# Performance work log

Hardware: AMD Instinct MI355X
Metric: run time of the kernel (lower is better)

The kernel has to match this reference:

```python
import jax, jax.numpy as jnp
import numpy as np

N, E, B = 50000, 800000, 64
IN_DIM, HID = 128, 64
H1 = 2  # heads in gat1
NEG_SLOPE = 0.2


def _glorot(key, shape):
    fan_in = shape[0]
    return jax.random.normal(key, shape, dtype=jnp.float32) / jnp.sqrt(jnp.float32(fan_in))


def setup_inputs() -> dict:
    key = jax.random.key(0)
    ks = jax.random.split(key, 24)
    x = jax.random.normal(ks[0], (N, IN_DIM), dtype=jnp.float32)
    edge_index = jax.random.randint(ks[1], (2, E), 0, N, dtype=jnp.int64)
    batch = jnp.sort(jax.random.randint(ks[2], (N,), 0, B, dtype=jnp.int64))
    d = {
        'x': x, 'edge_index': edge_index, 'batch': batch,
        # gat1: in=128 -> heads=2, out=64 (concat -> 128)
        'w1_l': _glorot(ks[3], (IN_DIM, H1 * HID)), 'b1_l': jnp.zeros((H1 * HID,), jnp.float32),
        'w1_r': _glorot(ks[4], (IN_DIM, H1 * HID)), 'b1_r': jnp.zeros((H1 * HID,), jnp.float32),
        'att1': _glorot(ks[5], (H1, HID)), 'bias1': jnp.zeros((H1 * HID,), jnp.float32),
        # gat2: in=128 -> heads=1, out=64
        'w2_l': _glorot(ks[6], (H1 * HID, HID)), 'b2_l': jnp.zeros((HID,), jnp.float32),
        'w2_r': _glorot(ks[7], (H1 * HID, HID)), 'b2_r': jnp.zeros((HID,), jnp.float32),
        'att2': _glorot(ks[8], (1, HID)), 'bias2': jnp.zeros((HID,), jnp.float32),
        # gate_nn: Linear(64,64) -> ReLU -> Linear(64,1)
        'gate_w1': _glorot(ks[9], (HID, HID)), 'gate_b1': jnp.zeros((HID,), jnp.float32),
        'gate_w2': _glorot(ks[10], (HID, 1)), 'gate_b2': jnp.zeros((1,), jnp.float32),
        # MLP head
        'lin1_w': _glorot(ks[11], (HID, HID)), 'lin1_b': jnp.zeros((HID,), jnp.float32),
        'lin2_w': _glorot(ks[12], (HID, 1)), 'lin2_b': jnp.zeros((1,), jnp.float32),
    }
    return d


def _segment_softmax(scores, seg, num_segments):
    # scores: [E, H]; softmax over edges sharing the same seg id (per column)
    m = jax.ops.segment_max(scores, seg, num_segments=num_segments)
    m = jnp.where(jnp.isfinite(m), m, 0.0)
    ex = jnp.exp(scores - m[seg])
    s = jax.ops.segment_sum(ex, seg, num_segments=num_segments)
    return ex / (s[seg] + 1e-16)


def _gatv2(x, src, dst, w_l, b_l, w_r, b_r, att, bias, heads, out_dim, n_nodes):
    xl = (x @ w_l + b_l).reshape(n_nodes, heads, out_dim)
    xr = (x @ w_r + b_r).reshape(n_nodes, heads, out_dim)
    e = jax.nn.leaky_relu(xl[src] + xr[dst], NEG_SLOPE)      # [E,H,D]
    score = jnp.einsum('ehd,hd->eh', e, att)                  # [E,H]
    alpha = _segment_softmax(score, dst, n_nodes)             # [E,H]
    out = jax.ops.segment_sum(alpha[..., None] * xl[src], dst, num_segments=n_nodes)
    return out.reshape(n_nodes, heads * out_dim) + bias


def reference(x, edge_index, batch, w1_l, b1_l, w1_r, b1_r, att1, bias1,
              w2_l, b2_l, w2_r, b2_r, att2, bias2,
              gate_w1, gate_b1, gate_w2, gate_b2,
              lin1_w, lin1_b, lin2_w, lin2_b):
    n = x.shape[0]
    # PyG GATv2Conv default add_self_loops=True
    loop = jnp.arange(n, dtype=edge_index.dtype)
    src = jnp.concatenate([edge_index[0], loop])
    dst = jnp.concatenate([edge_index[1], loop])

    h = jax.nn.relu(_gatv2(x, src, dst, w1_l, b1_l, w1_r, b1_r, att1, bias1, H1, HID, n))
    h = jax.nn.relu(_gatv2(h, src, dst, w2_l, b2_l, w2_r, b2_r, att2, bias2, 1, HID, n))

    # GlobalAttention pool: gate = gate_nn(h); softmax over batch; weighted sum
    gate = jax.nn.relu(h @ gate_w1 + gate_b1) @ gate_w2 + gate_b2     # [N,1]
    alpha = _segment_softmax(gate, batch, B)                           # [N,1]
    pooled = jax.ops.segment_sum(alpha * h, batch, num_segments=B)     # [B,HID]

    out = jax.nn.relu(pooled @ lin1_w + lin1_b)
    out = (out @ lin2_w + lin2_b).squeeze(-1)                          # [B]
    return out
```

## Files before the change

kernel.cpp:

```cpp
#include <hip/hip_runtime.h>

typedef float v2f __attribute__((ext_vector_type(2)));
typedef float v4f __attribute__((ext_vector_type(4)));
typedef _Float16 h4 __attribute__((ext_vector_type(4)));
typedef _Float16 f16x8 __attribute__((ext_vector_type(8)));

template<int N> struct IC { static constexpr int value = N; };


__global__ void k_init(const float* __restrict__ w1_l, const float* __restrict__ w1_r,
                       const float* __restrict__ b1_l, const float* __restrict__ b1_r,
                       const float* __restrict__ w2_l, const float* __restrict__ w2_r,
                       const float* __restrict__ b2_l, const float* __restrict__ b2_r,
                       _Float16* __restrict__ wc1h, _Float16* __restrict__ wc1l,
                       _Float16* __restrict__ wc2h, _Float16* __restrict__ wc2l,
                       float* __restrict__ bc1, float* __restrict__ bc2,
                       int* __restrict__ deg, int n){
  int i = blockIdx.x*256 + threadIdx.x;
  if (i < n) deg[i] = 0;
  if (i < 256*128){
    int col = i >> 7, k = i & 127;
    float v = (col < 128) ? w1_l[k*128 + col] : w1_r[k*128 + (col - 128)];
    _Float16 h = (_Float16)v;
    wc1h[i] = h; wc1l[i] = (_Float16)(v - (float)h);
  }
  if (i < 128*128){
    int col = i >> 7, k = i & 127;
    float v = (col < 64) ? w2_l[k*64 + col] : w2_r[k*64 + (col - 64)];
    _Float16 h = (_Float16)v;
    wc2h[i] = h; wc2l[i] = (_Float16)(v - (float)h);
  }
  if (i < 256) bc1[i] = (i < 128) ? b1_l[i] : b1_r[i - 128];
  if (i < 128) bc2[i] = (i < 64)  ? b2_l[i] : b2_r[i - 64];
}

__global__ void k_hist(const int* __restrict__ dstp, int* __restrict__ deg, int E){
  int e = blockIdx.x*256 + threadIdx.x;
  if (e < E) atomicAdd(&deg[dstp[e]], 1);
}

__global__ void k_scan1(const int* __restrict__ deg, int* __restrict__ rowptr,
                        int* __restrict__ bsum, int n){
  __shared__ int s[256];
  int i = blockIdx.x*256 + threadIdx.x;
  int v = (i < n) ? deg[i] + 1 : 0;
  s[threadIdx.x] = v;
  __syncthreads();
  for (int off = 1; off < 256; off <<= 1){
    int t = (threadIdx.x >= off) ? s[threadIdx.x - off] : 0;
    __syncthreads();
    s[threadIdx.x] += t;
    __syncthreads();
  }
  if (i < n) rowptr[i] = s[threadIdx.x] - v;
  if (threadIdx.x == 255) bsum[blockIdx.x] = s[255];
}

__global__ void k_scan2(int* bsum, int nb){
  __shared__ int s[256];
  int v = (threadIdx.x < nb) ? bsum[threadIdx.x] : 0;
  s[threadIdx.x] = v;
  __syncthreads();
  for (int off = 1; off < 256; off <<= 1){
    int t = (threadIdx.x >= off) ? s[threadIdx.x - off] : 0;
    __syncthreads();
    s[threadIdx.x] += t;
    __syncthreads();
  }
  if (threadIdx.x < nb) bsum[threadIdx.x] = s[threadIdx.x] - v;
}

__global__ void k_scan3(int* rowptr, const int* __restrict__ bsum,
                        int* __restrict__ srcs, int* __restrict__ cursor,
                        int n, int total){
  int i = blockIdx.x*256 + threadIdx.x;
  if (i < n){
    int b = rowptr[i] + bsum[blockIdx.x];
    rowptr[i] = b;
    srcs[b] = i;
    cursor[i] = b + 1;
  }
  if (i == 0) rowptr[n] = total;
}

__global__ void k_scatter(const int* __restrict__ srcp, const int* __restrict__ dstp,
                          int* __restrict__ cursor, int* __restrict__ srcs, int E){
  int e = blockIdx.x*256 + threadIdx.x;
  if (e < E){
    int p = atomicAdd(&cursor[dstp[e]], 1);
    srcs[p] = srcp[e];
  }
}


#define MBM 64
#define MBN 128
#define MBK 32

__device__ __forceinline__ int lds_idx(int row, int k){
  return row*32 + ((((k >> 3) ^ row) & 3) << 3) + (k & 7);
}

__global__ __launch_bounds__(256) void k_gemm_mfma(
    const float* __restrict__ A, const _Float16* __restrict__ Wh,
    const _Float16* __restrict__ Wl, const float* __restrict__ bias,
    _Float16* __restrict__ Cxl, float* __restrict__ Cxr,
    int M, int K, int N, int xlCols){
  __shared__ _Float16 Ah[MBM*MBK], Al[MBM*MBK];
  __shared__ _Float16 Bh[MBN*MBK], Bl[MBN*MBK];
  int bm = blockIdx.x * MBM, bn = blockIdx.y * MBN;
  int tid = threadIdx.x;
  int lane = tid & 63, wv = tid >> 6;
  v4f acc[8] = {};
  const int fragoff = (lane & 15)*32 + ((((lane >> 4) ^ lane) & 3) << 3);
  for (int k0 = 0; k0 < K; k0 += MBK){
    #pragma unroll
    for (int l = 0; l < 2; l++){
      int idx = tid + l*256;
      int r = idx >> 3, kq = (idx & 7) * 4;
      float4 v = make_float4(0.f, 0.f, 0.f, 0.f);
      if (bm + r < M) v = *(const float4*)(A + (size_t)(bm + r)*K + k0 + kq);
      _Float16 e0 = (_Float16)v.x, e1 = (_Float16)v.y,
               e2 = (_Float16)v.z, e3 = (_Float16)v.w;
      h4 hh = {e0, e1, e2, e3};
      h4 ll = {(_Float16)(v.x - (float)e0), (_Float16)(v.y - (float)e1),
               (_Float16)(v.z - (float)e2), (_Float16)(v.w - (float)e3)};
      int o = lds_idx(r, kq);
      *(h4*)(&Ah[o]) = hh;
      *(h4*)(&Al[o]) = ll;
    }
    #pragma unroll
    for (int l = 0; l < 2; l++){
      int idx = tid + l*256;
      int c = idx >> 2, kc = (idx & 3) * 8;
      size_t go = (size_t)(bn + c)*K + k0 + kc;
      int o = lds_idx(c, kc);
      *(f16x8*)(&Bh[o]) = *(const f16x8*)(Wh + go);
      *(f16x8*)(&Bl[o]) = *(const f16x8*)(Wl + go);
    }
    __syncthreads();
    f16x8 ah = *(const f16x8*)(&Ah[wv*16*32 + fragoff]);
    f16x8 al = *(const f16x8*)(&Al[wv*16*32 + fragoff]);
    #pragma unroll
    for (int t = 0; t < 8; t++){
      f16x8 bh = *(const f16x8*)(&Bh[t*16*32 + fragoff]);
      f16x8 bl = *(const f16x8*)(&Bl[t*16*32 + fragoff]);
      acc[t] = __builtin_amdgcn_mfma_f32_16x16x32_f16(ah, bh, acc[t], 0, 0, 0);
      acc[t] = __builtin_amdgcn_mfma_f32_16x16x32_f16(ah, bl, acc[t], 0, 0, 0);
      acc[t] = __builtin_amdgcn_mfma_f32_16x16x32_f16(al, bh, acc[t], 0, 0, 0);
    }
    __syncthreads();
  }
  int rbase = bm + wv*16 + (lane >> 4)*4;
  int cl = lane & 15;
  int NR = N - xlCols;
  #pragma unroll
  for (int t = 0; t < 8; t++){
    int col = bn + t*16 + cl;
    float bv = bias[col];
    bool isXl = (bn + t*16) < xlCols;
    #pragma unroll
    for (int i = 0; i < 4; i++){
      int r = rbase + i;
      if (r < M){
        float o = acc[t][i] + bv;
        if (isXl) Cxl[(size_t)r*xlCols + col] = (_Float16)o;
        else      Cxr[(size_t)r*NR + (col - xlCols)] = o;
      }
    }
  }
}


template<int CTRL>
__device__ __forceinline__ float dpp_add(float x){
  int t = __builtin_amdgcn_update_dpp(0, __float_as_int(x), CTRL, 0xf, 0xf, true);
  return x + __int_as_float(t);
}


template<int H>
__global__ __launch_bounds__(256) void k_gat_fused(
    const _Float16* __restrict__ xlh, const float* __restrict__ xr,
    const int* __restrict__ rowptr, const int* __restrict__ srcs,
    const float* __restrict__ att, const float* __restrict__ bias,
    float* __restrict__ out, int n){
  int gid = blockIdx.x * blockDim.x + threadIdx.x;
  int nd = gid >> 6, lane = gid & 63;
  if (nd >= n) return;
  constexpr int SHIFTB = (H == 2) ? 8 : 7;
  constexpr int EPI = (H == 2) ? 2 : 4;
  const int q = lane & 15;
  const int hsel = (H == 2) ? ((lane >> 4) & 1) : 0;
  const int elane = (H == 2) ? (lane >> 5) : (lane >> 4);
  const int fpos = hsel*64 + q*4;
  const unsigned foff = (unsigned)fpos * 2u;
  const char* __restrict__ xbase = (const char*)xlh;
  v4f xrv = *(const v4f*)(xr + (size_t)nd*(H*64) + fpos);
  v4f av  = *(const v4f*)(att + fpos);
  v4f acc = {0.f, 0.f, 0.f, 0.f};
  float den = 0.f;
  int s0 = rowptr[nd], s1 = rowptr[nd+1];
  for (int base = s0; base < s1; base += 64){
    int idx = base + lane;
    int sv = (idx < s1) ? srcs[idx] : 0;
    int cnt = min(64, s1 - base);
    auto batchU = [&](int i, auto Uc, bool full){
      constexpr int U = decltype(Uc)::value;
      int aidx[U];
      h4 hv[U];
      #pragma unroll
      for (int u = 0; u < U; u++)
        aidx[u] = __builtin_amdgcn_ds_bpermute((i + u*EPI + elane) << 2, sv);
      #pragma unroll
      for (int u = 0; u < U; u++)
        hv[u] = *(const h4*)(xbase + (((unsigned)aidx[u] << SHIFTB) + foff));
      #pragma unroll
      for (int u = 0; u < U; u++){
        v4f xv = {(float)hv[u].x, (float)hv[u].y, (float)hv[u].z, (float)hv[u].w};
        v4f t  = xv + xrv;
        v4f lt = __builtin_elementwise_max(t, t * 0.2f);
        v4f pr = lt * av;
        float p = (pr.x + pr.y) + (pr.z + pr.w);
        p = dpp_add<0x111>(p);
        p = dpp_add<0x112>(p);
        p = dpp_add<0x114>(p);
        p = dpp_add<0x118>(p);
        p = __int_as_float(__builtin_amdgcn_ds_swizzle(__float_as_int(p), 0x1F0));
        float ex = __expf(p);
        if (!full) ex = (elane < cnt - (i + u*EPI)) ? ex : 0.f;
        den += ex;
        acc += xv * ex;
      }
    };
    int i = 0;
    for (; i + 8*EPI <= cnt; i += 8*EPI) batchU(i, IC<8>{}, true);
    if (i + 4*EPI <= cnt){ batchU(i, IC<4>{}, true); i += 4*EPI; }
    if (i + 2*EPI <= cnt){ batchU(i, IC<2>{}, true); i += 2*EPI; }
    for (; i < cnt; i += EPI) batchU(i, IC<1>{}, i + EPI <= cnt);
  }
  if (H == 1){
    den   += __shfl_xor(den,   16, 64);
    acc.x += __shfl_xor(acc.x, 16, 64);
    acc.y += __shfl_xor(acc.y, 16, 64);
    acc.z += __shfl_xor(acc.z, 16, 64);
    acc.w += __shfl_xor(acc.w, 16, 64);
  }
  den   += __shfl_xor(den,   32, 64);
  acc.x += __shfl_xor(acc.x, 32, 64);
  acc.y += __shfl_xor(acc.y, 32, 64);
  acc.z += __shfl_xor(acc.z, 32, 64);
  acc.w += __shfl_xor(acc.w, 32, 64);
  if (lane < 16*H){
    v4f bv = *(const v4f*)(bias + lane*4);
    float inv = 1.f / (den + 1e-16f);
    v4f o = acc * inv + bv;
    v4f z = {0.f, 0.f, 0.f, 0.f};
    o = __builtin_elementwise_max(o, z);
    *(v4f*)(out + (size_t)nd*(H*64) + lane*4) = o;
  }
}


__global__ __launch_bounds__(256) void k_gate(
    const float* __restrict__ h2, const float* __restrict__ gw1,
    const float* __restrict__ gb1, const float* __restrict__ gw2,
    const float* __restrict__ gb2, float* __restrict__ exn, int M){
  __shared__ float As[32][64 + 4];
  __shared__ float Ws[32][64];
  int bm = blockIdx.x * 64;
  int tid = threadIdx.x;
  int tx = tid & 15, ty = tid >> 4;
  float acc[4][4] = {};
  for (int k0 = 0; k0 < 64; k0 += 32){
    #pragma unroll
    for (int l = 0; l < 2; l++){
      int idx = tid + l*256;
      int r = idx >> 3, c4 = (idx & 7) * 4;
      float4 v = make_float4(0.f, 0.f, 0.f, 0.f);
      if (bm + r < M) v = *(const float4*)(h2 + (size_t)(bm + r)*64 + k0 + c4);
      As[c4+0][r] = v.x; As[c4+1][r] = v.y; As[c4+2][r] = v.z; As[c4+3][r] = v.w;
      int kr = idx >> 4, wc4 = (idx & 15) * 4;
      *(float4*)(&Ws[kr][wc4]) = *(const float4*)(gw1 + (size_t)(k0 + kr)*64 + wc4);
    }
    __syncthreads();
    #pragma unroll
    for (int k = 0; k < 32; k++){
      float4 a4 = *(const float4*)(&As[k][ty*4]);
      float4 w4 = *(const float4*)(&Ws[k][tx*4]);
      float av[4] = {a4.x, a4.y, a4.z, a4.w};
      float wv[4] = {w4.x, w4.y, w4.z, w4.w};
      #pragma unroll
      for (int i = 0; i < 4; i++)
        #pragma unroll
        for (int j = 0; j < 4; j++)
          acc[i][j] = fmaf(av[i], wv[j], acc[i][j]);
    }
    __syncthreads();
  }
  float4 b4 = *(const float4*)(gb1 + tx*4);
  float4 w2 = *(const float4*)(gw2 + tx*4);
  float gb2v = gb2[0];
  #pragma unroll
  for (int i = 0; i < 4; i++){
    float p = fmaxf(acc[i][0] + b4.x, 0.f) * w2.x;
    p = fmaf(fmaxf(acc[i][1] + b4.y, 0.f), w2.y, p);
    p = fmaf(fmaxf(acc[i][2] + b4.z, 0.f), w2.z, p);
    p = fmaf(fmaxf(acc[i][3] + b4.w, 0.f), w2.w, p);
    p = dpp_add<0x111>(p);
    p = dpp_add<0x112>(p);
    p = dpp_add<0x114>(p);
    p = dpp_add<0x118>(p);
    if (tx == 15){
      int r = bm + ty*4 + i;
      if (r < M) exn[r] = __expf(p + gb2v);
    }
  }
}


__global__ __launch_bounds__(1024) void k_pool_mlp(
    const float* __restrict__ h2, const float* __restrict__ exn,
    const int* __restrict__ batch, int n,
    const float* __restrict__ l1w, const float* __restrict__ l1b,
    const float* __restrict__ l2w, const float* __restrict__ l2b,
    float* __restrict__ out){
  __shared__ float accs[16][64];
  __shared__ float dens[16];
  int b = blockIdx.x;
  int tid = threadIdx.x, lane = tid & 63, wv = tid >> 6;
  int lo = 0, hi = n;
  while (lo < hi){ int m = (lo + hi) >> 1; if (batch[m] < b) lo = m + 1; else hi = m; }
  int start = lo;
  hi = n;
  while (lo < hi){ int m = (lo + hi) >> 1; if (batch[m] < b + 1) lo = m + 1; else hi = m; }
  int end = lo;
  float acc = 0.f, den = 0.f;
  for (int nd = start + wv; nd < end; nd += 16){
    float ex = exn[nd];
    den += ex;
    acc = fmaf(ex, h2[(size_t)nd*64 + lane], acc);
  }
  accs[wv][lane] = acc;
  if (lane == 0) dens[wv] = den;
  __syncthreads();
  if (wv == 0){
    float p = 0.f, d = 0.f;
    #pragma unroll
    for (int w = 0; w < 16; w++){ p += accs[w][lane]; d += dens[w]; }
    p = p / (d + 1e-16f);
    float t = l1b[lane];
    #pragma unroll
    for (int k = 0; k < 64; k++)
      t = fmaf(__shfl(p, k, 64), l1w[k*64 + lane], t);
    t = fmaxf(t, 0.f) * l2w[lane];
    #pragma unroll
    for (int off = 32; off; off >>= 1) t += __shfl_xor(t, off, 64);
    if (lane == 0) out[b] = t + l2b[0];
  }
}


extern "C" void kernel_launch(void* const* d_in, const int* in_sizes, int n_in,
                              void* d_out, int out_size, void* d_ws, size_t ws_size,
                              hipStream_t stream){
  const float* x    = (const float*)d_in[0];
  const int*   ei   = (const int*)  d_in[1];
  const int*   batch= (const int*)  d_in[2];
  const float* w1_l = (const float*)d_in[3];  const float* b1_l = (const float*)d_in[4];
  const float* w1_r = (const float*)d_in[5];  const float* b1_r = (const float*)d_in[6];
  const float* att1 = (const float*)d_in[7];  const float* bias1= (const float*)d_in[8];
  const float* w2_l = (const float*)d_in[9];  const float* b2_l = (const float*)d_in[10];
  const float* w2_r = (const float*)d_in[11]; const float* b2_r = (const float*)d_in[12];
  const float* att2 = (const float*)d_in[13]; const float* bias2= (const float*)d_in[14];
  const float* gw1  = (const float*)d_in[15]; const float* gb1  = (const float*)d_in[16];
  const float* gw2  = (const float*)d_in[17]; const float* gb2  = (const float*)d_in[18];
  const float* l1w  = (const float*)d_in[19]; const float* l1b  = (const float*)d_in[20];
  const float* l2w  = (const float*)d_in[21]; const float* l2b  = (const float*)d_in[22];

  const int n = in_sizes[0] / 128;
  const int E = in_sizes[1] / 2;
  const int Bb = out_size;
  const int Etot = E + n;
  const int* srcp = ei;
  const int* dstp = ei + E;

  char* wsbase = (char*)d_ws;
  size_t off = 0;
  auto alloc = [&](size_t bytes)->char*{
    char* p = wsbase + off;
    off = (off + bytes + 255) & ~(size_t)255;
    return p;
  };
  int*   deg    = (int*)  alloc((size_t)n*4);
  int*   rowptr = (int*)  alloc((size_t)(n+1)*4);
  int*   cursor = (int*)  alloc((size_t)n*4);
  int*   bsum   = (int*)  alloc(1024);
  int*   srcs   = (int*)  alloc((size_t)Etot*4);
  _Float16* wc1h = (_Float16*)alloc(256*128*2);
  _Float16* wc1l = (_Float16*)alloc(256*128*2);
  _Float16* wc2h = (_Float16*)alloc(128*128*2);
  _Float16* wc2l = (_Float16*)alloc(128*128*2);
  float* bc1    = (float*)alloc(256*4);
  float* bc2    = (float*)alloc(128*4);
  _Float16* xlh1 = (_Float16*)alloc((size_t)n*128*2);
  float* xr1    = (float*)alloc((size_t)n*128*4);
  float* h1     = (float*)alloc((size_t)n*128*4);
  _Float16* xlh2 = xlh1;
  float* xr2 = xr1;
  float* h2  = xr1 + (size_t)n*64;
  float* exn = h1;

  int nb = (n + 255) / 256;
  int eb = (E + 255) / 256;
  int ib = (((n > 32768) ? n : 32768) + 255) / 256;

  k_init<<<ib, 256, 0, stream>>>(w1_l, w1_r, b1_l, b1_r, w2_l, w2_r, b2_l, b2_r,
                                 wc1h, wc1l, wc2h, wc2l, bc1, bc2, deg, n);
  k_hist<<<eb, 256, 0, stream>>>(dstp, deg, E);
  k_scan1<<<nb, 256, 0, stream>>>(deg, rowptr, bsum, n);
  k_scan2<<<1, 256, 0, stream>>>(bsum, nb);
  k_scan3<<<nb, 256, 0, stream>>>(rowptr, bsum, srcs, cursor, n, Etot);
  k_scatter<<<eb, 256, 0, stream>>>(srcp, dstp, cursor, srcs, E);

  dim3 g1((n + MBM - 1)/MBM, 2);
  k_gemm_mfma<<<g1, 256, 0, stream>>>(x, wc1h, wc1l, bc1, xlh1, xr1, n, 128, 256, 128);
  long long thr = (long long)n * 64;
  int gatb = (int)((thr + 255)/256);
  k_gat_fused<2><<<gatb, 256, 0, stream>>>(xlh1, xr1, rowptr, srcs, att1, bias1, h1, n);

  dim3 g2((n + MBM - 1)/MBM, 1);
  k_gemm_mfma<<<g2, 256, 0, stream>>>(h1, wc2h, wc2l, bc2, xlh2, xr2, n, 128, 128, 64);
  k_gat_fused<1><<<gatb, 256, 0, stream>>>(xlh2, xr2, rowptr, srcs, att2, bias2, h2, n);

  k_gate<<<(n + 63)/64, 256, 0, stream>>>(h2, gw1, gb1, gw2, gb2, exn, n);

  k_pool_mlp<<<Bb, 1024, 0, stream>>>(h2, exn, batch, n, l1w, l1b, l2w, l2b, (float*)d_out);
}
```

Baseline: 349.8 us.

## Replace direct CSR edge scatter with two-pass bucketed binning by 64-node groups

The single random-atomic scatter of edges into CSR slots is split into two passes. The first bins edges into 64-node buckets as packed (dst,src) pairs using per-bucket cursors. The second processes each bucket in its own block, where the per-node atomics and writes hit a small, cache-local region. This aims to cut scattered atomics and writes across the whole node range, at the cost of an extra kernel launch and an extra 8-byte-per-edge round trip through memory.

Measured after the change: 513.6 us. +46.8%, slower.

```diff
diff --git a/kernel.cpp b/kernel.cpp
--- a/kernel.cpp
+++ b/kernel.cpp
@@ -72,23 +72,42 @@
 
 __global__ void k_scan3(int* rowptr, const int* __restrict__ bsum,
                         int* __restrict__ srcs, int* __restrict__ cursor,
-                        int n, int total){
+                        int* __restrict__ bcur, int n, int total){
   int i = blockIdx.x*256 + threadIdx.x;
   if (i < n){
     int b = rowptr[i] + bsum[blockIdx.x];
     rowptr[i] = b;
     srcs[b] = i;
     cursor[i] = b + 1;
+    if ((i & 63) == 0) bcur[i >> 6] = b - i;
   }
   if (i == 0) rowptr[n] = total;
 }
 
-__global__ void k_scatter(const int* __restrict__ srcp, const int* __restrict__ dstp,
-                          int* __restrict__ cursor, int* __restrict__ srcs, int E){
+__global__ void k_bin(const int* __restrict__ srcp, const int* __restrict__ dstp,
+                      int* __restrict__ bcur, long long* __restrict__ pairs, int E){
   int e = blockIdx.x*256 + threadIdx.x;
   if (e < E){
-    int p = atomicAdd(&cursor[dstp[e]], 1);
-    srcs[p] = srcp[e];
+    int s = srcp[e], d = dstp[e];
+    int p = atomicAdd(&bcur[d >> 6], 1);
+    pairs[p] = ((long long)d << 32) | (unsigned)s;
+  }
+}
+
+__global__ void k_scatter2(const long long* __restrict__ pairs,
+                           const int* __restrict__ rowptr,
+                           int* __restrict__ cursor, int* __restrict__ srcs, int n){
+  int bk = blockIdx.x;
+  int n0 = bk << 6;
+  int n1 = min(n, n0 + 64);
+  int e0 = rowptr[n0] - n0;
+  int e1 = rowptr[n1] - n1;
+  for (int e = e0 + threadIdx.x; e < e1; e += 256){
+    long long pr = pairs[e];
+    int s = (int)(pr & 0xffffffffLL);
+    int d = (int)(pr >> 32);
+    int p = atomicAdd(&cursor[d], 1);
+    srcs[p] = s;
   }
 }
 
@@ -396,7 +415,9 @@
   int*   rowptr = (int*)  alloc((size_t)(n+1)*4);
   int*   cursor = (int*)  alloc((size_t)n*4);
   int*   bsum   = (int*)  alloc(1024);
+  int*   bcur   = (int*)  alloc((size_t)(((n+63)>>6)+1)*4);
   int*   srcs   = (int*)  alloc((size_t)Etot*4);
+  long long* pairs = (long long*)alloc((size_t)E*8);
   _Float16* wc1h = (_Float16*)alloc(256*128*2);
   _Float16* wc1l = (_Float16*)alloc(256*128*2);
   _Float16* wc2h = (_Float16*)alloc(128*128*2);
@@ -413,6 +434,7 @@
 
   int nb = (n + 255) / 256;
   int eb = (E + 255) / 256;
+  int nbk = (n + 63) >> 6;
   int ib = (((n > 32768) ? n : 32768) + 255) / 256;
 
   k_init<<<ib, 256, 0, stream>>>(w1_l, w1_r, b1_l, b1_r, w2_l, w2_r, b2_l, b2_r,
@@ -420,8 +442,9 @@
   k_hist<<<eb, 256, 0, stream>>>(dstp, deg, E);
   k_scan1<<<nb, 256, 0, stream>>>(deg, rowptr, bsum, n);
   k_scan2<<<1, 256, 0, stream>>>(bsum, nb);
-  k_scan3<<<nb, 256, 0, stream>>>(rowptr, bsum, srcs, cursor, n, Etot);
-  k_scatter<<<eb, 256, 0, stream>>>(srcp, dstp, cursor, srcs, E);
+  k_scan3<<<nb, 256, 0, stream>>>(rowptr, bsum, srcs, cursor, bcur, n, Etot);
+  k_bin<<<eb, 256, 0, stream>>>(srcp, dstp, bcur, pairs, E);
+  k_scatter2<<<nbk, 256, 0, stream>>>(pairs, rowptr, cursor, srcs, n);
 
   dim3 g1((n + MBM - 1)/MBM, 2);
   k_gemm_mfma<<<g1, 256, 0, stream>>>(x, wc1h, wc1l, bc1, xlh1, xr1, n, 128, 256, 128);
```
